# Optimization experiments

Hardware: AMD Instinct MI355X
Metric: run time of the kernel (lower is better)

Reference implementation:

```python
import jax, jax.numpy as jnp
import numpy as np

N = 40000   # entities
R = 200     # relations
T = 250000  # train edges (one direction)
E = 2 * T + N  # fwd + reverse + self-loops
D0, D = 100, 200   # init_emb_size, embedding_dim (= gc1_emb_size)
C, K = 128, 5      # conv channels, kernel size
B = 2048           # query batch
EPS = 1e-5


def setup_inputs() -> dict:
    key = jax.random.key(0)
    ks = jax.random.split(key, 24)
    def nrm(k, shape, s=0.05):
        return jax.random.normal(k, shape, jnp.float32) * s
    def bnp(k, dim):  # [gamma, beta, running_mean, running_var] stacked -> [4, dim]
        g = 1.0 + nrm(k, (dim,))
        b = nrm(jax.random.fold_in(k, 1), (dim,))
        m = nrm(jax.random.fold_in(k, 2), (dim,))
        v = 1.0 + 0.1 * jax.random.uniform(jax.random.fold_in(k, 3), (dim,), jnp.float32)
        return jnp.stack([g, b, m, v])
    inp = dict(
        src=jax.random.randint(ks[0], (E,), 0, N),
        dst=jax.random.randint(ks[1], (E,), 0, N),
        all_edge_type=jax.random.randint(ks[2], (E,), 0, R + 1),
        e1=jax.random.randint(ks[3], (B, 1), 0, N),
        rel=jax.random.randint(ks[4], (B, 1), 0, R),
        entity_id=jnp.arange(N),
        emb_e_w=nrm(ks[5], (N, D0), 0.1).at[0].set(0.0),   # padding_idx=0
        emb_rel_w=nrm(ks[6], (R, D), 0.1).at[0].set(0.0),
        w2=nrm(ks[7], (D0, D)), b2=nrm(ks[8], (D,)),
        alpha2=nrm(ks[9], (R + 1, 1)).at[0].set(0.0),
        w3=nrm(ks[10], (D, D)), b3=nrm(ks[11], (D,)),
        alpha3=nrm(ks[12], (R + 1, 1)).at[0].set(0.0),
        bn3=bnp(ks[13], D), bn4=bnp(ks[14], D),
        bn0=bnp(ks[15], 2), bn1=bnp(ks[16], C), bn2=bnp(ks[17], D),
        conv_w=nrm(ks[18], (C, 2, K)), conv_b=nrm(ks[19], (C,)),
        fc_w=nrm(ks[20], (D, D * C), 0.01), fc_b=nrm(ks[21], (D,)),
    )
    return inp


def _bn(x, p):  # eval-mode BatchNorm1d over last dim; p: [4, dim]
    g, b, m, v = p[0], p[1], p[2], p[3]
    return g * (x - m) * jax.lax.rsqrt(v + EPS) + b


def _bn_ch(x, p):  # x: [B, C, L]; normalize over channel dim
    g, b, m, v = (p[i][None, :, None] for i in range(4))
    return g * (x - m) * jax.lax.rsqrt(v + EPS) + b


def _gcn(x, w, b, alpha, src, dst, alp_types, alp_types_t, n):
    feats = x @ w                                   # [N, out]
    alp = alpha[alp_types] + alpha[alp_types_t]     # [E, 1]
    out = jax.ops.segment_sum(feats[src] * alp, dst, num_segments=n)
    return out + b


def reference(src, dst, all_edge_type, e1, rel, entity_id,
              emb_e_w, emb_rel_w, w2, b2, alpha2, w3, b3, alpha3,
              bn3, bn4, bn0, bn1, bn2, conv_w, conv_b, fc_w, fc_b):
    n = entity_id.shape[0]
    t = (all_edge_type.shape[0] - n) // 2
    # transpose edge types: [reverse, forward, self-loops]
    types_t = jnp.concatenate([all_edge_type[t:2 * t], all_edge_type[:t], all_edge_type[2 * t:]])

    x = emb_e_w[entity_id]                                   # [N, D0]
    x = _gcn(x, w2, b2, alpha2, src, dst, all_edge_type, types_t, n)
    x = jnp.tanh(_bn(x, bn3))                                # dropout: eval -> identity
    x = _gcn(x, w3, b3, alpha3, src, dst, all_edge_type, types_t, n)
    x = jnp.tanh(_bn(x, bn4))                                # final_bn + final_act
    e_all = x                                                # [N, D]

    e1_emb = e_all[e1]                                       # [B, 1, D]
    rel_emb = emb_rel_w[rel]                                 # [B, 1, D]
    h = jnp.concatenate([e1_emb, rel_emb], axis=1)           # [B, 2, D]
    h = _bn_ch(h, bn0)
    h = jax.lax.conv_general_dilated(h, conv_w, (1,), [(K // 2, K // 2)],
                                     dimension_numbers=('NCH', 'OIH', 'NCH'))
    h = h + conv_b[None, :, None]                            # [B, C, D]
    h = jax.nn.relu(_bn_ch(h, bn1))
    h = h.reshape(h.shape[0], -1)                            # [B, C*D]
    h = h @ fc_w.T + fc_b                                    # [B, D]
    h = jax.nn.relu(_bn(h, bn2))
    return jax.nn.sigmoid(h @ e_all.T)                       # [B, N]
```

## Files before the change

kernel.cpp:

```cpp
#include <hip/hip_runtime.h>
#include <math.h>

#define NENT 40000
#define NTE  250000
#define NE   540000
#define DIM0 100
#define DIM  200
#define CCH  128
#define BQ   2048
#define FCK  25600
#define EPSB 1e-5f
#define KPAD 224
#define EMBS 104

typedef float f32x4 __attribute__((ext_vector_type(4)));
typedef _Float16 h8 __attribute__((ext_vector_type(8)));
typedef _Float16 h4 __attribute__((ext_vector_type(4)));

__global__ void k_hist(const int* __restrict__ dst, int* __restrict__ deg) {
    int e = blockIdx.x * 256 + threadIdx.x;
    if (e < NE) atomicAdd(&deg[dst[e]], 1);
}

__global__ __launch_bounds__(1024) void k_scan(const int* __restrict__ deg,
        int* __restrict__ rowptr, int* __restrict__ cursor) {
    __shared__ int sums[1024];
    int t = threadIdx.x;
    int base = t * 40;
    int local[40];
    int s = 0;
    #pragma unroll
    for (int i = 0; i < 40; i++) {
        int idx = base + i;
        int v = (idx < NENT) ? deg[idx] : 0;
        local[i] = s;
        s += v;
    }
    sums[t] = s;
    __syncthreads();
    #pragma unroll
    for (int off = 1; off < 1024; off <<= 1) {
        int add = (t >= off) ? sums[t - off] : 0;
        __syncthreads();
        sums[t] += add;
        __syncthreads();
    }
    int prefix = (t == 0) ? 0 : sums[t - 1];
    #pragma unroll
    for (int i = 0; i < 40; i++) {
        int idx = base + i;
        if (idx < NENT) {
            int p = prefix + local[i];
            rowptr[idx] = p;
            cursor[idx] = p;
        }
    }
    if (t == 1023) rowptr[NENT] = prefix + s;
}

__global__ void k_scatter(const int* __restrict__ src, const int* __restrict__ dst,
                          const int* __restrict__ aet, const float* __restrict__ a2t,
                          const float* __restrict__ a3t, int* __restrict__ cursor,
                          int* __restrict__ ssrc, float* __restrict__ sa1,
                          float* __restrict__ sa2) {
    int e = blockIdx.x * 256 + threadIdx.x;
    if (e >= NE) return;
    int tt = (e < NTE) ? e + NTE : (e < 2 * NTE ? e - NTE : e);
    int t0 = aet[e], t1 = aet[tt];
    int pos = atomicAdd(&cursor[dst[e]], 1);
    ssrc[pos] = src[e];
    sa1[pos] = a2t[t0] + a2t[t1];
    sa2[pos] = a3t[t0] + a3t[t1];
}

template<int NL, int NPADL, int SS, int OS>
__global__ __launch_bounds__(256) void k_agg_raw(const int* __restrict__ rowptr,
        const int* __restrict__ ssrc, const float* __restrict__ sa,
        const _Float16* __restrict__ srcd, _Float16* __restrict__ outd) {
    int w = threadIdx.x >> 6, l = threadIdx.x & 63;
    int row = blockIdx.x * 4 + w;
    int beg = rowptr[row], end = rowptr[row + 1];
    bool act = l < NL;
    int col = l * 4;
    float sx = 0.f, sy = 0.f, sz = 0.f, sw = 0.f;
    int i = beg;
    for (; i + 4 <= end; i += 4) {
        int i0 = ssrc[i], i1 = ssrc[i + 1], i2 = ssrc[i + 2], i3 = ssrc[i + 3];
        float a0 = sa[i], a1 = sa[i + 1], a2 = sa[i + 2], a3 = sa[i + 3];
        if (act) {
            h4 v0 = *(const h4*)(srcd + (long)i0 * SS + col);
            h4 v1 = *(const h4*)(srcd + (long)i1 * SS + col);
            h4 v2 = *(const h4*)(srcd + (long)i2 * SS + col);
            h4 v3 = *(const h4*)(srcd + (long)i3 * SS + col);
            sx += a0 * (float)v0[0] + a1 * (float)v1[0] + a2 * (float)v2[0] + a3 * (float)v3[0];
            sy += a0 * (float)v0[1] + a1 * (float)v1[1] + a2 * (float)v2[1] + a3 * (float)v3[1];
            sz += a0 * (float)v0[2] + a1 * (float)v1[2] + a2 * (float)v2[2] + a3 * (float)v3[2];
            sw += a0 * (float)v0[3] + a1 * (float)v1[3] + a2 * (float)v2[3] + a3 * (float)v3[3];
        }
    }
    for (; i < end; i++) {
        int i0 = ssrc[i];
        float a0 = sa[i];
        if (act) {
            h4 v0 = *(const h4*)(srcd + (long)i0 * SS + col);
            sx += a0 * (float)v0[0]; sy += a0 * (float)v0[1];
            sz += a0 * (float)v0[2]; sw += a0 * (float)v0[3];
        }
    }
    if (act) {
        h4 o = { (_Float16)sx, (_Float16)sy, (_Float16)sz, (_Float16)sw };
        *(h4*)(outd + (long)row * OS + col) = o;
    } else if (l < NPADL) {
        h4 z = { (_Float16)0.f, (_Float16)0.f, (_Float16)0.f, (_Float16)0.f };
        *(h4*)(outd + (long)row * OS + col) = z;
    }
}

__global__ void k_pack_emb(const float* __restrict__ emb, const int* __restrict__ ent,
                           _Float16* __restrict__ o) {
    long i = (long)blockIdx.x * 256 + threadIdx.x;
    if (i >= (long)NENT * 13) return;
    long m = i / 13;
    int k0 = (int)(i % 13) * 8;
    h8 h = {};
    const float* p = emb + (long)ent[m] * DIM0 + k0;
    #pragma unroll
    for (int j = 0; j < 8; j++)
        if (k0 + j < DIM0) h[j] = (_Float16)p[j];
    *(h8*)(o + m * EMBS + k0) = h;
}

__global__ void k_pack_B16(const float* __restrict__ w, _Float16* __restrict__ bf,
                           int kin, int kpad, int nrows) {
    int i = blockIdx.x * 256 + threadIdx.x;
    if (i >= nrows * kpad) return;
    int k = i % kpad, n = i / kpad;
    bf[i] = (k < kin && n < DIM) ? (_Float16)w[(long)k * DIM + n] : (_Float16)0.f;
}

__global__ void k_hq16(const int* __restrict__ e1, const int* __restrict__ rel,
                       const _Float16* __restrict__ ef, const float* __restrict__ embrel,
                       const float* __restrict__ bn0, _Float16* __restrict__ hq) {
    int i = blockIdx.x * 256 + threadIdx.x;
    if (i >= BQ * 2 * DIM) return;
    int d = i % DIM, c = (i / DIM) & 1, b = i / (2 * DIM);
    float val = (c == 0) ? (float)ef[(long)e1[b] * KPAD + d]
                         : embrel[(long)rel[b] * DIM + d];
    float g = bn0[c], be = bn0[2 + c], m = bn0[4 + c], v = bn0[6 + c];
    hq[i] = (_Float16)(g * (val - m) * rsqrtf(v + EPSB) + be);
}

__global__ void k_pack_fcw(const float* __restrict__ w, _Float16* __restrict__ wf) {
    long i = (long)blockIdx.x * 256 + threadIdx.x;
    if (i >= (long)208 * (FCK / 8)) return;
    int n = (int)(i / (FCK / 8));
    long k0 = (i % (FCK / 8)) * 8;
    h8 h = {};
    if (n < DIM) {
        const float* p = w + (long)n * FCK + k0;
        #pragma unroll
        for (int j = 0; j < 8; j++) h[j] = (_Float16)p[j];
    }
    *(h8*)(wf + (long)n * FCK + k0) = h;
}

template<int NT>
__global__ __launch_bounds__(256) void k_gemm16f(
        const _Float16* __restrict__ A, const _Float16* __restrict__ B,
        const float* __restrict__ bias, const float* __restrict__ bn,
        _Float16* __restrict__ C, int kpad, int ostride) {
    int w = threadIdx.x >> 6, l = threadIdx.x & 63;
    long m0 = (long)blockIdx.x * 64 + w * 16;
    long arow = m0 + (l & 15);
    int kg = (l >> 4) * 8;
    const _Float16* ap = A + arow * kpad + kg;
    f32x4 acc[NT];
    #pragma unroll
    for (int i = 0; i < NT; i++) acc[i] = (f32x4){0.f, 0.f, 0.f, 0.f};
    for (int kb = 0; kb < kpad; kb += 32) {
        h8 a = *(const h8*)(ap + kb);
        #pragma unroll
        for (int nt = 0; nt < NT; nt++) {
            h8 b = *(const h8*)(B + (long)(nt * 16 + (l & 15)) * kpad + kb + kg);
            acc[nt] = __builtin_amdgcn_mfma_f32_16x16x32_f16(a, b, acc[nt], 0, 0, 0);
        }
    }
    long rowo = m0 + (l >> 4) * 4;
    #pragma unroll
    for (int nt = 0; nt < NT; nt++) {
        int col = nt * 16 + (l & 15);
        if (col < ostride) {
            _Float16 vals[4];
            if (col < DIM) {
                float g = bn[col], be = bn[DIM + col], m = bn[2 * DIM + col],
                      v = bn[3 * DIM + col], bb = bias[col];
                float sc = g * rsqrtf(v + EPSB);
                #pragma unroll
                for (int rr = 0; rr < 4; rr++)
                    vals[rr] = (_Float16)tanhf(sc * (acc[nt][rr] + bb - m) + be);
            } else {
                #pragma unroll
                for (int rr = 0; rr < 4; rr++) vals[rr] = (_Float16)0.f;
            }
            #pragma unroll
            for (int rr = 0; rr < 4; rr++)
                C[(rowo + rr) * ostride + col] = vals[rr];
        }
    }
}

__global__ __launch_bounds__(256) void k_convfc(
        const _Float16* __restrict__ hq16, const float* __restrict__ convw,
        const float* __restrict__ convb, const float* __restrict__ bn1,
        const _Float16* __restrict__ B, float* __restrict__ fcsum) {
    __shared__ _Float16 ldsA[64][40];
    __shared__ _Float16 ldsB[208][40];
    __shared__ float cwl[4][12];
    int bid = blockIdx.y * 8 + blockIdx.x;
    int wsw = (bid & 7) * 128 + (bid >> 3);
    int mb = wsw & 31, split = wsw >> 5;
    int t = threadIdx.x;
    int w = t >> 6, l = t & 63;
    int kbase = split * 800;
    int c0 = split * 4;
    if (t < 40) cwl[t / 10][t % 10] = convw[(c0 + t / 10) * 10 + t % 10];
    if (t < 4) {
        int c = c0 + t;
        float g = bn1[c], be = bn1[CCH + c], m = bn1[2 * CCH + c], v = bn1[3 * CCH + c];
        float s = g * rsqrtf(v + EPSB);
        cwl[t][10] = s;
        cwl[t][11] = be - m * s + s * convb[c];
    }
    __syncthreads();

    int r = t >> 2, q = t & 3;
    const _Float16* hrow = hq16 + (long)(mb * 64 + r) * 400;

    h8 z = {};
    h8 v0a, v1a, v2a, v0b, v1b, v2b;
    {
        int p = q * 8;
        v0a = (p >= 8) ? *(const h8*)(hrow + p - 8) : z;
        v1a = *(const h8*)(hrow + p);
        v2a = (p + 8 < DIM) ? *(const h8*)(hrow + p + 8) : z;
        v0b = (p >= 8) ? *(const h8*)(hrow + DIM + p - 8) : z;
        v1b = *(const h8*)(hrow + DIM + p);
        v2b = (p + 8 < DIM) ? *(const h8*)(hrow + DIM + p + 8) : z;
    }
    h8 bR[4];
    #pragma unroll
    for (int i2 = 0; i2 < 4; i2++) {
        int u = i2 * 256 + t;
        bR[i2] = (u < 832) ? *(const h8*)(B + (long)(u >> 2) * FCK + kbase + (u & 3) * 8) : z;
    }

    f32x4 acc[13];
    #pragma unroll
    for (int i = 0; i < 13; i++) acc[i] = (f32x4){0.f, 0.f, 0.f, 0.f};

    for (int ks = 0; ks < 25; ks++) {
        int off = ks * 32 + q * 8;
        int cl = off / 200;
        float cwv[12];
        #pragma unroll
        for (int k2 = 0; k2 < 12; k2++) cwv[k2] = cwl[cl][k2];
        float wa[12], wb[12];
        wa[0] = (float)v0a[6]; wa[1] = (float)v0a[7];
        wb[0] = (float)v0b[6]; wb[1] = (float)v0b[7];
        #pragma unroll
        for (int m2 = 0; m2 < 8; m2++) {
            wa[2 + m2] = (float)v1a[m2];
            wb[2 + m2] = (float)v1b[m2];
        }
        wa[10] = (float)v2a[0]; wa[11] = (float)v2a[1];
        wb[10] = (float)v2b[0]; wb[11] = (float)v2b[1];
        h8 aOut;
        #pragma unroll
        for (int j = 0; j < 8; j++) {
            float s = 0.f;
            #pragma unroll
            for (int kk = 0; kk < 5; kk++)
                s += wa[j + kk] * cwv[kk] + wb[j + kk] * cwv[5 + kk];
            aOut[j] = (_Float16)fmaxf(cwv[10] * s + cwv[11], 0.f);
        }
        *(h8*)&ldsA[r][q * 8] = aOut;
        #pragma unroll
        for (int i2 = 0; i2 < 4; i2++) {
            int u = i2 * 256 + t;
            if (u < 832) *(h8*)&ldsB[u >> 2][(u & 3) * 8] = bR[i2];
        }
        __syncthreads();
        if (ks + 1 < 25) {
            int off1 = (ks + 1) * 32 + q * 8;
            int cl1 = off1 / 200;
            int p1 = off1 - cl1 * 200;
            v0a = (p1 >= 8) ? *(const h8*)(hrow + p1 - 8) : z;
            v1a = *(const h8*)(hrow + p1);
            v2a = (p1 + 8 < DIM) ? *(const h8*)(hrow + p1 + 8) : z;
            v0b = (p1 >= 8) ? *(const h8*)(hrow + DIM + p1 - 8) : z;
            v1b = *(const h8*)(hrow + DIM + p1);
            v2b = (p1 + 8 < DIM) ? *(const h8*)(hrow + DIM + p1 + 8) : z;
            int knext = kbase + (ks + 1) * 32;
            #pragma unroll
            for (int i2 = 0; i2 < 4; i2++) {
                int u = i2 * 256 + t;
                if (u < 832) bR[i2] = *(const h8*)(B + (long)(u >> 2) * FCK + knext + (u & 3) * 8);
            }
        }
        h8 a = *(const h8*)&ldsA[w * 16 + (l & 15)][(l >> 4) * 8];
        #pragma unroll
        for (int nt = 0; nt < 13; nt++) {
            h8 b = *(const h8*)&ldsB[nt * 16 + (l & 15)][(l >> 4) * 8];
            acc[nt] = __builtin_amdgcn_mfma_f32_16x16x32_f16(a, b, acc[nt], 0, 0, 0);
        }
        __syncthreads();
    }
    long rowo = mb * 64 + w * 16 + (l >> 4) * 4;
    #pragma unroll
    for (int nt = 0; nt < 13; nt++) {
        int col = nt * 16 + (l & 15);
        if (col < DIM) {
            #pragma unroll
            for (int rr = 0; rr < 4; rr++)
                unsafeAtomicAdd(&fcsum[(rowo + rr) * DIM + col], acc[nt][rr]);
        }
    }
}

__global__ void k_fcreduce(const float* __restrict__ fcsum, const float* __restrict__ fcb,
                           const float* __restrict__ bn2, _Float16* __restrict__ h3) {
    int i = blockIdx.x * 256 + threadIdx.x;
    if (i >= BQ * KPAD) return;
    int j = i % KPAD, b = i / KPAD;
    _Float16 o = (_Float16)0.f;
    if (j < DIM) {
        float s = fcsum[(long)b * DIM + j] + fcb[j];
        float g = bn2[j], be = bn2[DIM + j], m = bn2[2 * DIM + j], v = bn2[3 * DIM + j];
        s = g * (s - m) * rsqrtf(v + EPSB) + be;
        o = (_Float16)fmaxf(s, 0.f);
    }
    h3[i] = o;
}

__global__ __launch_bounds__(256) void k_mfma_final(
        const _Float16* __restrict__ A, const _Float16* __restrict__ B,
        float* __restrict__ out) {
    __shared__ float tl[4][32][68];
    int bid = blockIdx.y * 8 + blockIdx.x;
    int wsw = (bid & 7) * 625 + (bid >> 3);
    int mbb = wsw & 7, nbb = wsw >> 3;
    int w = threadIdx.x >> 6, l = threadIdx.x & 63;
    int n0 = nbb * 64;
    int m0 = mbb * 256 + w * 64;
    int lr = l & 15;
    int kb = (l >> 4) * 8;
    const _Float16* aph = A + (long)(m0 + lr) * KPAD + kb;
    const _Float16* bph = B + (long)(n0 + lr) * KPAD + kb;
    h8 ac[4], bc[4], an[4], bn_[4];
    #pragma unroll
    for (int x = 0; x < 4; x++) {
        ac[x] = *(const h8*)(aph + (long)x * 16 * KPAD);
        bc[x] = *(const h8*)(bph + (long)x * 16 * KPAD);
    }
    f32x4 acc[4][4];
    #pragma unroll
    for (int i = 0; i < 4; i++)
        #pragma unroll
        for (int j = 0; j < 4; j++) acc[i][j] = (f32x4){0.f, 0.f, 0.f, 0.f};
    for (int kt = 0; kt < 7; kt++) {
        int ko = kt * 32 + 32;
        if (kt < 6) {
            #pragma unroll
            for (int x = 0; x < 4; x++) {
                an[x]  = *(const h8*)(aph + (long)x * 16 * KPAD + ko);
                bn_[x] = *(const h8*)(bph + (long)x * 16 * KPAD + ko);
            }
        }
        #pragma unroll
        for (int mt = 0; mt < 4; mt++)
            #pragma unroll
            for (int nt = 0; nt < 4; nt++)
                acc[mt][nt] = __builtin_amdgcn_mfma_f32_16x16x32_f16(ac[mt], bc[nt], acc[mt][nt], 0, 0, 0);
        if (kt < 6) {
            #pragma unroll
            for (int x = 0; x < 4; x++) { ac[x] = an[x]; bc[x] = bn_[x]; }
        }
    }
    #pragma unroll
    for (int hh = 0; hh < 2; hh++) {
        #pragma unroll
        for (int mt2 = 0; mt2 < 2; mt2++) {
            int mt = hh * 2 + mt2;
            #pragma unroll
            for (int nt = 0; nt < 4; nt++)
                #pragma unroll
                for (int r = 0; r < 4; r++)
                    tl[w][mt2 * 16 + (l >> 4) * 4 + r][nt * 16 + lr] = acc[mt][nt][r];
        }
        #pragma unroll
        for (int i = 0; i < 8; i++) {
            int rr = i * 4 + (l >> 4);
            f32x4 v = *(const f32x4*)&tl[w][rr][lr * 4];
            f32x4 o;
            o.x = __builtin_amdgcn_rcpf(1.f + __expf(-v.x));
            o.y = __builtin_amdgcn_rcpf(1.f + __expf(-v.y));
            o.z = __builtin_amdgcn_rcpf(1.f + __expf(-v.z));
            o.w = __builtin_amdgcn_rcpf(1.f + __expf(-v.w));
            long row = m0 + hh * 32 + rr;
            __builtin_nontemporal_store(o, (f32x4*)&out[row * NENT + n0 + lr * 4]);
        }
    }
}

extern "C" void kernel_launch(void* const* d_in, const int* in_sizes, int n_in,
                              void* d_out, int out_size, void* d_ws, size_t ws_size,
                              hipStream_t stream) {
    (void)in_sizes; (void)n_in; (void)out_size; (void)ws_size;
    const int* src      = (const int*)d_in[0];
    const int* dst      = (const int*)d_in[1];
    const int* aet      = (const int*)d_in[2];
    const int* e1       = (const int*)d_in[3];
    const int* rel      = (const int*)d_in[4];
    const int* entity   = (const int*)d_in[5];
    const float* emb_e  = (const float*)d_in[6];
    const float* embrel = (const float*)d_in[7];
    const float* w2     = (const float*)d_in[8];
    const float* b2     = (const float*)d_in[9];
    const float* alpha2 = (const float*)d_in[10];
    const float* w3     = (const float*)d_in[11];
    const float* b3     = (const float*)d_in[12];
    const float* alpha3 = (const float*)d_in[13];
    const float* bn3    = (const float*)d_in[14];
    const float* bn4    = (const float*)d_in[15];
    const float* bn0    = (const float*)d_in[16];
    const float* bn1    = (const float*)d_in[17];
    const float* bn2    = (const float*)d_in[18];
    const float* convw  = (const float*)d_in[19];
    const float* convb  = (const float*)d_in[20];
    const float* fcw    = (const float*)d_in[21];
    const float* fcb    = (const float*)d_in[22];
    float* out = (float*)d_out;
    float* ws = (float*)d_ws;

    _Float16* emb16 = (_Float16*)ws;
    _Float16* aggE  = (_Float16*)(ws + 3000000);
    _Float16* x1_f  = (_Float16*)(ws + 6000000);
    _Float16* aggX  = (_Float16*)(ws + 11000000);
    _Float16* e_f   = (_Float16*)(ws + 16000000);
    _Float16* fcw_f = (_Float16*)(ws + 21000000);
    _Float16* hq16  = (_Float16*)(ws + 24000000);
    int*   deg    = (int*)(ws + 51000000);
    int*   rowptr = (int*)(ws + 51050000);
    int*   cursor = (int*)(ws + 51100000);
    int*   ssrc   = (int*)(ws + 51200000);
    float* sa1    = ws + 51800000;
    float* sa2    = ws + 52400000;
    float* fcsum  = ws + 53000000;
    _Float16* h3_f  = (_Float16*)(ws + 54400000);
    _Float16* w2t_f = (_Float16*)(ws + 54700000);
    _Float16* w3t_f = (_Float16*)(ws + 54750000);

    hipMemsetAsync(deg, 0, NENT * 4, stream);
    k_hist<<<(NE + 255) / 256, 256, 0, stream>>>(dst, deg);
    k_scan<<<1, 1024, 0, stream>>>(deg, rowptr, cursor);
    k_scatter<<<(NE + 255) / 256, 256, 0, stream>>>(src, dst, aet, alpha2, alpha3,
                                                    cursor, ssrc, sa1, sa2);

    k_pack_emb<<<(NENT * 13 + 255) / 256, 256, 0, stream>>>(emb_e, entity, emb16);
    k_pack_B16<<<(208 * 128 + 255) / 256, 256, 0, stream>>>(w2, w2t_f, DIM0, 128, 208);
    k_pack_B16<<<(224 * KPAD + 255) / 256, 256, 0, stream>>>(w3, w3t_f, DIM, KPAD, 224);

    k_agg_raw<26, 32, EMBS, 128><<<NENT / 4, 256, 0, stream>>>(rowptr, ssrc, sa1,
                                                               emb16, aggE);
    k_gemm16f<13><<<NENT / 64, 256, 0, stream>>>(aggE, w2t_f, b2, bn3, x1_f, 128, DIM);

    k_agg_raw<50, 56, DIM, KPAD><<<NENT / 4, 256, 0, stream>>>(rowptr, ssrc, sa2,
                                                               x1_f, aggX);
    k_gemm16f<14><<<NENT / 64, 256, 0, stream>>>(aggX, w3t_f, b3, bn4, e_f, KPAD, KPAD);

    k_hq16<<<(BQ * 2 * DIM + 255) / 256, 256, 0, stream>>>(e1, rel, e_f, embrel, bn0, hq16);
    k_pack_fcw<<<(int)(((long)208 * (FCK / 8) + 255) / 256), 256, 0, stream>>>(fcw, fcw_f);

    hipMemsetAsync(fcsum, 0, (size_t)BQ * DIM * 4, stream);
    k_convfc<<<dim3(8, 128), 256, 0, stream>>>(hq16, convw, convb, bn1, fcw_f, fcsum);
    k_fcreduce<<<(BQ * KPAD + 255) / 256, 256, 0, stream>>>(fcsum, fcb, bn2, h3_f);

    k_mfma_final<<<dim3(8, NENT / 64), 256, 0, stream>>>(h3_f, e_f, out);
}
```

Before: 518.3 us.

## Fuse prep/pack kernels into one launch and shrink final GEMM M-tile

Combines the degree/fcsum zeroing and the embedding, weight and fc-weight fp16 packing into a single multi-section kernel indexed by blockIdx.y, removing several launches and memsets. The final scoring GEMM now uses 128-row blocks (32 rows per wave) instead of 256, doubling the grid and halving accumulator registers so more waves can be resident and hide the latency of the large output stores. The trade-off is more redundant loads of the entity-embedding tiles across blocks.

```diff
diff --git a/kernel.cpp b/kernel.cpp
--- a/kernel.cpp
+++ b/kernel.cpp
@@ -16,6 +16,55 @@
 typedef float f32x4 __attribute__((ext_vector_type(4)));
 typedef _Float16 h8 __attribute__((ext_vector_type(8)));
 typedef _Float16 h4 __attribute__((ext_vector_type(4)));
+
+__global__ __launch_bounds__(256) void k_prep(
+        const float* __restrict__ emb, const int* __restrict__ ent,
+        const float* __restrict__ w2, const float* __restrict__ w3,
+        const float* __restrict__ fcw,
+        int* __restrict__ deg, float* __restrict__ fcsum,
+        _Float16* __restrict__ emb16, _Float16* __restrict__ w2t,
+        _Float16* __restrict__ w3t, _Float16* __restrict__ fcwf) {
+    long i = (long)blockIdx.x * 256 + threadIdx.x;
+    int sec = blockIdx.y;
+    if (sec == 0) {
+        if (i < NENT) deg[i] = 0;
+    } else if (sec == 1) {
+        if (i < BQ * DIM) fcsum[i] = 0.f;
+    } else if (sec == 2) {
+        if (i < (long)NENT * 13) {
+            long m = i / 13;
+            int k0 = (int)(i % 13) * 8;
+            h8 h = {};
+            const float* p = emb + (long)ent[m] * DIM0 + k0;
+            #pragma unroll
+            for (int j = 0; j < 8; j++)
+                if (k0 + j < DIM0) h[j] = (_Float16)p[j];
+            *(h8*)(emb16 + m * EMBS + k0) = h;
+        }
+    } else if (sec == 3) {
+        if (i < 208 * 128) {
+            int k = (int)(i % 128), n = (int)(i / 128);
+            w2t[i] = (k < DIM0 && n < DIM) ? (_Float16)w2[(long)k * DIM + n] : (_Float16)0.f;
+        }
+    } else if (sec == 4) {
+        if (i < 224 * KPAD) {
+            int k = (int)(i % KPAD), n = (int)(i / KPAD);
+            w3t[i] = (k < DIM && n < DIM) ? (_Float16)w3[(long)k * DIM + n] : (_Float16)0.f;
+        }
+    } else {
+        if (i < (long)208 * (FCK / 8)) {
+            int n = (int)(i / (FCK / 8));
+            long k0 = (i % (FCK / 8)) * 8;
+            h8 h = {};
+            if (n < DIM) {
+                const float* p = fcw + (long)n * FCK + k0;
+                #pragma unroll
+                for (int j = 0; j < 8; j++) h[j] = (_Float16)p[j];
+            }
+            *(h8*)(fcwf + (long)n * FCK + k0) = h;
+        }
+    }
+}
 
 __global__ void k_hist(const int* __restrict__ dst, int* __restrict__ deg) {
     int e = blockIdx.x * 256 + threadIdx.x;
@@ -116,28 +165,6 @@
     }
 }
 
-__global__ void k_pack_emb(const float* __restrict__ emb, const int* __restrict__ ent,
-                           _Float16* __restrict__ o) {
-    long i = (long)blockIdx.x * 256 + threadIdx.x;
-    if (i >= (long)NENT * 13) return;
-    long m = i / 13;
-    int k0 = (int)(i % 13) * 8;
-    h8 h = {};
-    const float* p = emb + (long)ent[m] * DIM0 + k0;
-    #pragma unroll
-    for (int j = 0; j < 8; j++)
-        if (k0 + j < DIM0) h[j] = (_Float16)p[j];
-    *(h8*)(o + m * EMBS + k0) = h;
-}
-
-__global__ void k_pack_B16(const float* __restrict__ w, _Float16* __restrict__ bf,
-                           int kin, int kpad, int nrows) {
-    int i = blockIdx.x * 256 + threadIdx.x;
-    if (i >= nrows * kpad) return;
-    int k = i % kpad, n = i / kpad;
-    bf[i] = (k < kin && n < DIM) ? (_Float16)w[(long)k * DIM + n] : (_Float16)0.f;
-}
-
 __global__ void k_hq16(const int* __restrict__ e1, const int* __restrict__ rel,
                        const _Float16* __restrict__ ef, const float* __restrict__ embrel,
                        const float* __restrict__ bn0, _Float16* __restrict__ hq) {
@@ -148,20 +175,6 @@
                          : embrel[(long)rel[b] * DIM + d];
     float g = bn0[c], be = bn0[2 + c], m = bn0[4 + c], v = bn0[6 + c];
     hq[i] = (_Float16)(g * (val - m) * rsqrtf(v + EPSB) + be);
-}
-
-__global__ void k_pack_fcw(const float* __restrict__ w, _Float16* __restrict__ wf) {
-    long i = (long)blockIdx.x * 256 + threadIdx.x;
-    if (i >= (long)208 * (FCK / 8)) return;
-    int n = (int)(i / (FCK / 8));
-    long k0 = (i % (FCK / 8)) * 8;
-    h8 h = {};
-    if (n < DIM) {
-        const float* p = w + (long)n * FCK + k0;
-        #pragma unroll
-        for (int j = 0; j < 8; j++) h[j] = (_Float16)p[j];
-    }
-    *(h8*)(wf + (long)n * FCK + k0) = h;
 }
 
 template<int NT>
@@ -347,68 +360,67 @@
         float* __restrict__ out) {
     __shared__ float tl[4][32][68];
     int bid = blockIdx.y * 8 + blockIdx.x;
-    int wsw = (bid & 7) * 625 + (bid >> 3);
-    int mbb = wsw & 7, nbb = wsw >> 3;
+    int wsw = (bid & 7) * 1250 + (bid >> 3);
+    int mbb = wsw & 15, nbb = wsw >> 4;
     int w = threadIdx.x >> 6, l = threadIdx.x & 63;
     int n0 = nbb * 64;
-    int m0 = mbb * 256 + w * 64;
+    int m0 = mbb * 128 + w * 32;
     int lr = l & 15;
     int kb = (l >> 4) * 8;
     const _Float16* aph = A + (long)(m0 + lr) * KPAD + kb;
     const _Float16* bph = B + (long)(n0 + lr) * KPAD + kb;
-    h8 ac[4], bc[4], an[4], bn_[4];
-    #pragma unroll
-    for (int x = 0; x < 4; x++) {
+    h8 ac[2], bc[4], an[2], bn_[4];
+    #pragma unroll
+    for (int x = 0; x < 2; x++)
         ac[x] = *(const h8*)(aph + (long)x * 16 * KPAD);
+    #pragma unroll
+    for (int x = 0; x < 4; x++)
         bc[x] = *(const h8*)(bph + (long)x * 16 * KPAD);
-    }
-    f32x4 acc[4][4];
-    #pragma unroll
-    for (int i = 0; i < 4; i++)
+    f32x4 acc[2][4];
+    #pragma unroll
+    for (int i = 0; i < 2; i++)
         #pragma unroll
         for (int j = 0; j < 4; j++) acc[i][j] = (f32x4){0.f, 0.f, 0.f, 0.f};
     for (int kt = 0; kt < 7; kt++) {
         int ko = kt * 32 + 32;
         if (kt < 6) {
             #pragma unroll
-            for (int x = 0; x < 4; x++) {
-                an[x]  = *(const h8*)(aph + (long)x * 16 * KPAD + ko);
+            for (int x = 0; x < 2; x++)
+                an[x] = *(const h8*)(aph + (long)x * 16 * KPAD + ko);
+            #pragma unroll
+            for (int x = 0; x < 4; x++)
                 bn_[x] = *(const h8*)(bph + (long)x * 16 * KPAD + ko);
-            }
-        }
-        #pragma unroll
-        for (int mt = 0; mt < 4; mt++)
+        }
+        #pragma unroll
+        for (int mt = 0; mt < 2; mt++)
             #pragma unroll
             for (int nt = 0; nt < 4; nt++)
                 acc[mt][nt] = __builtin_amdgcn_mfma_f32_16x16x32_f16(ac[mt], bc[nt], acc[mt][nt], 0, 0, 0);
         if (kt < 6) {
             #pragma unroll
-            for (int x = 0; x < 4; x++) { ac[x] = an[x]; bc[x] = bn_[x]; }
-        }
-    }
-    #pragma unroll
-    for (int hh = 0; hh < 2; hh++) {
-        #pragma unroll
-        for (int mt2 = 0; mt2 < 2; mt2++) {
-            int mt = hh * 2 + mt2;
-            #pragma unroll
-            for (int nt = 0; nt < 4; nt++)
-                #pragma unroll
-                for (int r = 0; r < 4; r++)
-                    tl[w][mt2 * 16 + (l >> 4) * 4 + r][nt * 16 + lr] = acc[mt][nt][r];
-        }
-        #pragma unroll
-        for (int i = 0; i < 8; i++) {
-            int rr = i * 4 + (l >> 4);
-            f32x4 v = *(const f32x4*)&tl[w][rr][lr * 4];
-            f32x4 o;
-            o.x = __builtin_amdgcn_rcpf(1.f + __expf(-v.x));
-            o.y = __builtin_amdgcn_rcpf(1.f + __expf(-v.y));
-            o.z = __builtin_amdgcn_rcpf(1.f + __expf(-v.z));
-            o.w = __builtin_amdgcn_rcpf(1.f + __expf(-v.w));
-            long row = m0 + hh * 32 + rr;
-            __builtin_nontemporal_store(o, (f32x4*)&out[row * NENT + n0 + lr * 4]);
-        }
+            for (int x = 0; x < 2; x++) ac[x] = an[x];
+            #pragma unroll
+            for (int x = 0; x < 4; x++) bc[x] = bn_[x];
+        }
+    }
+    #pragma unroll
+    for (int mt = 0; mt < 2; mt++)
+        #pragma unroll
+        for (int nt = 0; nt < 4; nt++)
+            #pragma unroll
+            for (int r = 0; r < 4; r++)
+                tl[w][mt * 16 + (l >> 4) * 4 + r][nt * 16 + lr] = acc[mt][nt][r];
+    #pragma unroll
+    for (int i = 0; i < 8; i++) {
+        int rr = i * 4 + (l >> 4);
+        f32x4 v = *(const f32x4*)&tl[w][rr][lr * 4];
+        f32x4 o;
+        o.x = __builtin_amdgcn_rcpf(1.f + __expf(-v.x));
+        o.y = __builtin_amdgcn_rcpf(1.f + __expf(-v.y));
+        o.z = __builtin_amdgcn_rcpf(1.f + __expf(-v.z));
+        o.w = __builtin_amdgcn_rcpf(1.f + __expf(-v.w));
+        long row = m0 + rr;
+        __builtin_nontemporal_store(o, (f32x4*)&out[row * NENT + n0 + lr * 4]);
     }
 }
 
@@ -460,16 +472,14 @@
     _Float16* w2t_f = (_Float16*)(ws + 54700000);
     _Float16* w3t_f = (_Float16*)(ws + 54750000);
 
-    hipMemsetAsync(deg, 0, NENT * 4, stream);
+    k_prep<<<dim3(2600, 6), 256, 0, stream>>>(emb_e, entity, w2, w3, fcw,
+                                              deg, fcsum, emb16, w2t_f, w3t_f, fcw_f);
+
     k_hist<<<(NE + 255) / 256, 256, 0, stream>>>(dst, deg);
     k_scan<<<1, 1024, 0, stream>>>(deg, rowptr, cursor);
     k_scatter<<<(NE + 255) / 256, 256, 0, stream>>>(src, dst, aet, alpha2, alpha3,
                                                     cursor, ssrc, sa1, sa2);
 
-    k_pack_emb<<<(NENT * 13 + 255) / 256, 256, 0, stream>>>(emb_e, entity, emb16);
-    k_pack_B16<<<(208 * 128 + 255) / 256, 256, 0, stream>>>(w2, w2t_f, DIM0, 128, 208);
-    k_pack_B16<<<(224 * KPAD + 255) / 256, 256, 0, stream>>>(w3, w3t_f, DIM, KPAD, 224);
-
     k_agg_raw<26, 32, EMBS, 128><<<NENT / 4, 256, 0, stream>>>(rowptr, ssrc, sa1,
                                                                emb16, aggE);
     k_gemm16f<13><<<NENT / 64, 256, 0, stream>>>(aggE, w2t_f, b2, bn3, x1_f, 128, DIM);
@@ -479,11 +489,9 @@
     k_gemm16f<14><<<NENT / 64, 256, 0, stream>>>(aggX, w3t_f, b3, bn4, e_f, KPAD, KPAD);
 
     k_hq16<<<(BQ * 2 * DIM + 255) / 256, 256, 0, stream>>>(e1, rel, e_f, embrel, bn0, hq16);
-    k_pack_fcw<<<(int)(((long)208 * (FCK / 8) + 255) / 256), 256, 0, stream>>>(fcw, fcw_f);
-
-    hipMemsetAsync(fcsum, 0, (size_t)BQ * DIM * 4, stream);
+
     k_convfc<<<dim3(8, 128), 256, 0, stream>>>(hq16, convw, convb, bn1, fcw_f, fcsum);
     k_fcreduce<<<(BQ * KPAD + 255) / 256, 256, 0, stream>>>(fcsum, fcb, bn2, h3_f);
 
-    k_mfma_final<<<dim3(8, NENT / 64), 256, 0, stream>>>(h3_f, e_f, out);
-}
+    k_mfma_final<<<dim3(8, 1250), 256, 0, stream>>>(h3_f, e_f, out);
+}
```

Measured after the change: 536.0 us. 1.03x slower.
